# Kernel optimization log

Measured on AMD Instinct MI355X. Metric: run time of the kernel, lower is better.

Reference implementation:

```python
import jax, jax.numpy as jnp
import numpy as np

B, H, S, D = 4, 16, 2048, 64

def setup_inputs() -> dict:
    key = jax.random.key(0)
    kq, kk, kv = jax.random.split(key, 3)
    Q = jax.random.normal(kq, (B, H, S, D), dtype=jnp.float32)
    K = jax.random.normal(kk, (B, H, S, D), dtype=jnp.float32)
    V = jax.random.normal(kv, (B, H, S, D), dtype=jnp.float32)
    return {"Q": Q, "K": K, "V": V}

def reference(Q, K, V):
    d = Q.shape[-1]
    scale = jnp.sqrt(jnp.asarray(d, dtype=Q.dtype))
    # scores: [B, H, S, S]
    scores = jnp.einsum('bhqd,bhkd->bhqk', Q, K) / scale
    attn = jax.nn.softmax(scores, axis=-1)
    out = jnp.einsum('bhqk,bhkd->bhqd', attn, V)  # [B,H,S,D]
    # permute to [B,S,H,D] then merge heads -> [B,S,H*D]
    b, h, s, dd = out.shape
    return out.transpose(0, 2, 1, 3).reshape(b, s, h * dd)
```

## Files before the change

### kernel.cpp

```cpp
#include <hip/hip_runtime.h>
#include <hip/hip_bf16.h>


#define B_ 4
#define H_ 16
#define S_ 2048
#define D_ 64
#define BH 64
#define NKT 32
#define TILE_USH 4096
#define ARR_USH ((size_t)BH * NKT * TILE_USH)
#define WS_NEED (2 * ARR_USH * 2)
#define QSCALE 0.18033688011112042f

typedef float  f4 __attribute__((ext_vector_type(4)));
typedef short  s4 __attribute__((ext_vector_type(4)));
typedef short  s8 __attribute__((ext_vector_type(8)));
typedef unsigned short ushort_t;

__device__ __forceinline__ unsigned short f2bf(float x) {
  unsigned int u = __float_as_uint(x);
  u += 0x7fffu + ((u >> 16) & 1u);
  return (unsigned short)(u >> 16);
}
__device__ __forceinline__ unsigned int pk_bf16(float a, float b) {
  __hip_bfloat162 h = __float22bfloat162_rn(make_float2(a, b));
  union { __hip_bfloat162 h2; unsigned int u; } cv; cv.h2 = h; return cv.u;
}
__device__ __forceinline__ void splitbf_rne(float x, unsigned short& hi, unsigned short& lo) {
  hi = f2bf(x);
  float hf = __uint_as_float((unsigned int)hi << 16);
  lo = f2bf(x - hf);
}
__device__ __forceinline__ void splitbf(float x, unsigned short& hi, unsigned short& lo) {
  unsigned int u = __float_as_uint(x);
  hi = (unsigned short)(u >> 16);
  float hf = __uint_as_float(u & 0xffff0000u);
  lo = (unsigned short)(__float_as_uint(x - hf) >> 16);
}

typedef __attribute__((address_space(1))) const unsigned int* gas_t;
typedef __attribute__((address_space(3))) unsigned int* las_t;
__device__ __forceinline__ void gl_lds16(const void* g, void* l) {
  __builtin_amdgcn_global_load_lds((gas_t)g, (las_t)l, 16, 0, 0);
}

__global__ __launch_bounds__(256)
void prep(const float* __restrict__ K, const float* __restrict__ V,
          ushort_t* __restrict__ KH, ushort_t* __restrict__ VT) {
  __shared__ float Vf[64][68];
  const int tile = blockIdx.x;
  const int t = threadIdx.x;

  const float* vsrc = V + (size_t)tile * 4096;
  float4 vv[4];
  int srow[4], dcol[4];
  #pragma unroll
  for (int r = 0; r < 4; ++r) {
    int f = r * 256 + t; srow[r] = f >> 4; dcol[r] = (f & 15) << 2;
    vv[r] = *(const float4*)(vsrc + srow[r] * 64 + dcol[r]);
  }
  {
    const float* src0 = K + (size_t)tile * 4096;
    #pragma unroll
    for (int u = 0; u < 2; ++u) {
      unsigned int i = u * 256 + t;
      unsigned int row = i >> 3, c = (i & 7) ^ (row & 7);
      const float* src = src0 + row * 64 + c * 8;
      float4 a = *(const float4*)src;
      float4 b = *(const float4*)(src + 4);
      unsigned int d0 = pk_bf16(a.x, a.y), d1 = pk_bf16(a.z, a.w);
      unsigned int d2 = pk_bf16(b.x, b.y), d3 = pk_bf16(b.z, b.w);
      uint4 out = make_uint4(d0, d1, d2, d3);
      *(uint4*)(KH + (size_t)tile * TILE_USH + i * 8) = out;
    }
  }
  #pragma unroll
  for (int r = 0; r < 4; ++r) {
    int pcol = dcol[r] ^ (((srow[r] >> 3) & 3) << 2);
    *(float4*)&Vf[srow[r]][pcol] = vv[r];
  }
  __syncthreads();
  #pragma unroll
  for (int u = 0; u < 2; ++u) {
    unsigned int i = u * 256 + t;
    unsigned int drow = i >> 3, c = (i & 7) ^ (drow & 7);
    const unsigned int col = drow ^ ((c & 3) << 2);
    unsigned int d0 = pk_bf16(Vf[c * 8 + 0][col], Vf[c * 8 + 1][col]);
    unsigned int d1 = pk_bf16(Vf[c * 8 + 2][col], Vf[c * 8 + 3][col]);
    unsigned int d2 = pk_bf16(Vf[c * 8 + 4][col], Vf[c * 8 + 5][col]);
    unsigned int d3 = pk_bf16(Vf[c * 8 + 6][col], Vf[c * 8 + 7][col]);
    uint4 out = make_uint4(d0, d1, d2, d3);
    *(uint4*)(VT + (size_t)tile * TILE_USH + i * 8) = out;
  }
}

__global__ __launch_bounds__(256, 2)
void attn6(const float* __restrict__ Q, const ushort_t* __restrict__ KH,
           const ushort_t* __restrict__ VT, float* __restrict__ O) {
  __shared__ ushort_t KhS[2][TILE_USH];
  __shared__ ushort_t VtS[2][TILE_USH];
  __shared__ ushort_t Pb[4][TILE_USH];

  const int t    = threadIdx.x;
  const int w    = t >> 6;
  const int lane = t & 63;
  const int g    = lane >> 4;
  const int ln   = lane & 15;

  const unsigned int n = blockIdx.x;
  const int bh = (int)((n >> 6) * 8 + (n & 7));
  const int q0 = (int)(((n >> 3) & 7) * 256);

  const size_t tb = (size_t)bh * NKT * TILE_USH;
  const unsigned int cb = w * 128;

  #pragma unroll
  for (int j = 0; j < 2; ++j) {
    const unsigned int ch = cb + 64u * j;
    const size_t go = tb + (size_t)(ch + lane) * 8;
    gl_lds16(KH + go, &KhS[0][ch * 8]);
    gl_lds16(VT + go, &VtS[0][ch * 8]);
  }

  s8 qfh[4][2], qfl[4][2];
  #pragma unroll
  for (int sub = 0; sub < 4; ++sub) {
    const int q = q0 + 64 * w + 16 * sub + ln;
    #pragma unroll
    for (int ks = 0; ks < 2; ++ks) {
      const float* qp = Q + ((size_t)bh * S_ + q) * 64 + 32 * ks + 8 * g;
      float4 a = *(const float4*)qp;
      float4 b = *(const float4*)(qp + 4);
      float xs[8] = {a.x, a.y, a.z, a.w, b.x, b.y, b.z, b.w};
      s8 hv, lv;
      #pragma unroll
      for (int j = 0; j < 8; ++j) {
        unsigned short h, lo; splitbf_rne(xs[j] * QSCALE, h, lo);
        hv[j] = (short)h; lv[j] = (short)lo;
      }
      qfh[sub][ks] = hv; qfl[sub][ks] = lv;
    }
  }

  f4 oacc[4][4];
  f4 lacc[4];
  #pragma unroll
  for (int s = 0; s < 4; ++s) {
    lacc[s] = (f4)0.0f;
    #pragma unroll
    for (int d = 0; d < 4; ++d) oacc[s][d] = (f4)0.0f;
  }

  s8 ones;
  #pragma unroll
  for (int j = 0; j < 8; ++j) ones[j] = (short)0x3F80;

  unsigned int foff[2];
  #pragma unroll
  for (int ks = 0; ks < 2; ++ks)
    foff[ks] = (unsigned)ln * 128u + (unsigned)(((4 * ks + g) ^ (ln & 7)) * 16);

  for (int kt = 0; kt < NKT; ++kt) {
    const int cur = kt & 1;
    __syncthreads();

    if (kt + 1 < NKT) {
      const size_t tbase = tb + (size_t)(kt + 1) * TILE_USH;
      const int nb = cur ^ 1;
      #pragma unroll
      for (int j = 0; j < 2; ++j) {
        const unsigned int ch = cb + 64u * j;
        const size_t go = tbase + (size_t)(ch + lane) * 8;
        gl_lds16(KH + go, &KhS[nb][ch * 8]);
        gl_lds16(VT + go, &VtS[nb][ch * 8]);
      }
    }

    const char* khb = (const char*)&KhS[cur][0];
    const char* vtb = (const char*)&VtS[cur][0];

    #pragma unroll
    for (int nt = 0; nt < 4; ++nt) {
      s8 kh0 = *(const s8*)(khb + nt * 2048 + foff[0]);
      s8 kh1 = *(const s8*)(khb + nt * 2048 + foff[1]);
      #pragma unroll
      for (int sub = 0; sub < 4; ++sub) {
        f4 sc = (f4)0.0f;
        sc = __builtin_amdgcn_mfma_f32_16x16x32_bf16(qfh[sub][0], kh0, sc, 0, 0, 0);
        sc = __builtin_amdgcn_mfma_f32_16x16x32_bf16(qfl[sub][0], kh0, sc, 0, 0, 0);
        sc = __builtin_amdgcn_mfma_f32_16x16x32_bf16(qfh[sub][1], kh1, sc, 0, 0, 0);
        sc = __builtin_amdgcn_mfma_f32_16x16x32_bf16(qfl[sub][1], kh1, sc, 0, 0, 0);
        float p0 = __builtin_amdgcn_exp2f(sc[0]);
        float p1 = __builtin_amdgcn_exp2f(sc[1]);
        float p2 = __builtin_amdgcn_exp2f(sc[2]);
        float p3 = __builtin_amdgcn_exp2f(sc[3]);
        unsigned int pk01 = pk_bf16(p0, p1);
        unsigned int pk23 = pk_bf16(p2, p3);
        const unsigned int c0 = 16u * nt + (unsigned)ln;
        ushort_t* base = &Pb[w][(16 * sub + 4 * g) * 64];
        base[       (c0 ^ (8u * (unsigned)((4 * g + 0) & 7)))] = (ushort_t)pk01;
        base[ 64u + (c0 ^ (8u * (unsigned)((4 * g + 1) & 7)))] = (ushort_t)(pk01 >> 16);
        base[128u + (c0 ^ (8u * (unsigned)((4 * g + 2) & 7)))] = (ushort_t)pk23;
        base[192u + (c0 ^ (8u * (unsigned)((4 * g + 3) & 7)))] = (ushort_t)(pk23 >> 16);
      }
    }

    #pragma unroll
    for (int ks = 0; ks < 2; ++ks) {
      s8 pa[4];
      #pragma unroll
      for (int sub = 0; sub < 4; ++sub) {
        pa[sub] = *(const s8*)((const char*)&Pb[w][0] + sub * 2048 + foff[ks]);
        lacc[sub] = __builtin_amdgcn_mfma_f32_16x16x32_bf16(pa[sub], ones, lacc[sub], 0, 0, 0);
      }
      #pragma unroll
      for (int dt = 0; dt < 4; ++dt) {
        s8 vb = *(const s8*)(vtb + dt * 2048 + foff[ks]);
        #pragma unroll
        for (int sub = 0; sub < 4; ++sub)
          oacc[sub][dt] = __builtin_amdgcn_mfma_f32_16x16x32_bf16(pa[sub], vb, oacc[sub][dt], 0, 0, 0);
      }
    }
  }

  const int b = bh >> 4, h = bh & 15;
  #pragma unroll
  for (int sub = 0; sub < 4; ++sub)
    #pragma unroll
    for (int r = 0; r < 4; ++r) {
      const float inv = 1.0f / lacc[sub][r];
      const int q = q0 + 64 * w + 16 * sub + 4 * g + r;
      float* dst = O + ((size_t)b * S_ + q) * (H_ * D_) + h * 64;
      #pragma unroll
      for (int dt = 0; dt < 4; ++dt)
        dst[16 * dt + ln] = oacc[sub][dt][r] * inv;
    }
}

#define KQ_STR 72
#define VP_STR 76
__global__ __launch_bounds__(256, 2)
void attn_mfma(const float* __restrict__ Q, const float* __restrict__ K,
               const float* __restrict__ V, float* __restrict__ O) {
  __shared__ __align__(16) unsigned short Qh[64][KQ_STR];
  __shared__ __align__(16) unsigned short Ql[64][KQ_STR];
  __shared__ __align__(16) unsigned short Kh[64][KQ_STR];
  __shared__ __align__(16) unsigned short Kl[64][KQ_STR];
  __shared__ __align__(16) unsigned short Vt[64][VP_STR];
  __shared__ __align__(16) unsigned short Pb2[4][16][VP_STR];
  const int t = threadIdx.x, w = t >> 6, lane = t & 63, g = lane >> 4, ln = lane & 15;
  const int bh = blockIdx.x, q0 = blockIdx.y * 64;
  const size_t base = (size_t)bh * S_ * D_;
  {
    const float* Qg = Q + base + (size_t)q0 * D_;
    #pragma unroll
    for (int r = 0; r < 4; ++r) {
      int f = r * 256 + t, row = f >> 4, c4 = (f & 15) << 2;
      float4 v = *(const float4*)(Qg + row * 64 + c4);
      s4 hv, lv; unsigned short hb, lb;
      splitbf(v.x * 0.125f, hb, lb); hv[0] = (short)hb; lv[0] = (short)lb;
      splitbf(v.y * 0.125f, hb, lb); hv[1] = (short)hb; lv[1] = (short)lb;
      splitbf(v.z * 0.125f, hb, lb); hv[2] = (short)hb; lv[2] = (short)lb;
      splitbf(v.w * 0.125f, hb, lb); hv[3] = (short)hb; lv[3] = (short)lb;
      *(s4*)&Qh[row][c4] = hv; *(s4*)&Ql[row][c4] = lv;
    }
  }
  __syncthreads();
  s8 qfh[2], qfl[2];
  #pragma unroll
  for (int ks = 0; ks < 2; ++ks) {
    qfh[ks] = *(const s8*)&Qh[16 * w + ln][ks * 32 + 8 * g];
    qfl[ks] = *(const s8*)&Ql[16 * w + ln][ks * 32 + 8 * g];
  }
  f4 oacc[4]; float m[4], l[4];
  #pragma unroll
  for (int i = 0; i < 4; ++i) { oacc[i] = (f4)0.0f; m[i] = -1e30f; l[i] = 0.0f; }
  const float* Kg = K + base; const float* Vg = V + base;
  float4 kreg[4], vreg[4];
  #pragma unroll
  for (int r = 0; r < 4; ++r) {
    int f = r * 256 + t, row = f >> 4, c4 = (f & 15) << 2;
    kreg[r] = *(const float4*)(Kg + row * 64 + c4);
  }
  #pragma unroll
  for (int j = 0; j < 2; ++j) {
    int it = j * 256 + t, kp = it >> 4, c4 = (it & 15) << 2;
    vreg[2 * j] = *(const float4*)(Vg + (2 * kp) * 64 + c4);
    vreg[2 * j + 1] = *(const float4*)(Vg + (2 * kp + 1) * 64 + c4);
  }
  for (int kt = 0; kt < S_ / 64; ++kt) {
    __syncthreads();
    #pragma unroll
    for (int r = 0; r < 4; ++r) {
      int f = r * 256 + t, row = f >> 4, c4 = (f & 15) << 2;
      float4 v = kreg[r];
      s4 hv, lv; unsigned short hb, lb;
      splitbf(v.x, hb, lb); hv[0] = (short)hb; lv[0] = (short)lb;
      splitbf(v.y, hb, lb); hv[1] = (short)hb; lv[1] = (short)lb;
      splitbf(v.z, hb, lb); hv[2] = (short)hb; lv[2] = (short)lb;
      splitbf(v.w, hb, lb); hv[3] = (short)hb; lv[3] = (short)lb;
      *(s4*)&Kh[row][c4] = hv; *(s4*)&Kl[row][c4] = lv;
    }
    #pragma unroll
    for (int j = 0; j < 2; ++j) {
      int it = j * 256 + t, kp = it >> 4, c4 = (it & 15) << 2;
      float4 a = vreg[2 * j], b = vreg[2 * j + 1];
      float xa[4] = {a.x, a.y, a.z, a.w}, xb[4] = {b.x, b.y, b.z, b.w};
      #pragma unroll
      for (int i = 0; i < 4; ++i) {
        unsigned int pk = (unsigned int)f2bf(xa[i]) | ((unsigned int)f2bf(xb[i]) << 16);
        *(unsigned int*)&Vt[c4 + i][2 * kp] = pk;
      }
    }
    if (kt + 1 < S_ / 64) {
      const float* Kt = Kg + (size_t)(kt + 1) * 4096;
      const float* Vn = Vg + (size_t)(kt + 1) * 4096;
      #pragma unroll
      for (int r = 0; r < 4; ++r) {
        int f = r * 256 + t, row = f >> 4, c4 = (f & 15) << 2;
        kreg[r] = *(const float4*)(Kt + row * 64 + c4);
      }
      #pragma unroll
      for (int j = 0; j < 2; ++j) {
        int it = j * 256 + t, kp = it >> 4, c4 = (it & 15) << 2;
        vreg[2 * j] = *(const float4*)(Vn + (2 * kp) * 64 + c4);
        vreg[2 * j + 1] = *(const float4*)(Vn + (2 * kp + 1) * 64 + c4);
      }
    }
    __syncthreads();
    f4 sacc[4];
    #pragma unroll
    for (int nt = 0; nt < 4; ++nt) sacc[nt] = (f4)0.0f;
    #pragma unroll
    for (int nt = 0; nt < 4; ++nt)
      #pragma unroll
      for (int ks = 0; ks < 2; ++ks) {
        s8 kh = *(const s8*)&Kh[16 * nt + ln][ks * 32 + 8 * g];
        s8 kl = *(const s8*)&Kl[16 * nt + ln][ks * 32 + 8 * g];
        sacc[nt] = __builtin_amdgcn_mfma_f32_16x16x32_bf16(qfh[ks], kh, sacc[nt], 0, 0, 0);
        sacc[nt] = __builtin_amdgcn_mfma_f32_16x16x32_bf16(qfl[ks], kh, sacc[nt], 0, 0, 0);
        sacc[nt] = __builtin_amdgcn_mfma_f32_16x16x32_bf16(qfh[ks], kl, sacc[nt], 0, 0, 0);
      }
    #pragma unroll
    for (int r = 0; r < 4; ++r) {
      float rm = fmaxf(fmaxf(sacc[0][r], sacc[1][r]), fmaxf(sacc[2][r], sacc[3][r]));
      rm = fmaxf(rm, __shfl_xor(rm, 1)); rm = fmaxf(rm, __shfl_xor(rm, 2));
      rm = fmaxf(rm, __shfl_xor(rm, 4)); rm = fmaxf(rm, __shfl_xor(rm, 8));
      float mn = fmaxf(m[r], rm);
      float alpha = __expf(m[r] - mn); m[r] = mn;
      float p0 = __expf(sacc[0][r] - mn), p1 = __expf(sacc[1][r] - mn);
      float p2 = __expf(sacc[2][r] - mn), p3 = __expf(sacc[3][r] - mn);
      float rs = p0 + p1 + p2 + p3;
      rs += __shfl_xor(rs, 1); rs += __shfl_xor(rs, 2);
      rs += __shfl_xor(rs, 4); rs += __shfl_xor(rs, 8);
      l[r] = l[r] * alpha + rs;
      oacc[0][r] *= alpha; oacc[1][r] *= alpha; oacc[2][r] *= alpha; oacc[3][r] *= alpha;
      const int row = 4 * g + r;
      Pb2[w][row][ln] = f2bf(p0); Pb2[w][row][ln + 16] = f2bf(p1);
      Pb2[w][row][ln + 32] = f2bf(p2); Pb2[w][row][ln + 48] = f2bf(p3);
    }
    #pragma unroll
    for (int ks = 0; ks < 2; ++ks) {
      s4 pa0 = *(const s4*)&Pb2[w][ln][ks * 32 + 8 * g];
      s4 pa1 = *(const s4*)&Pb2[w][ln][ks * 32 + 8 * g + 4];
      s8 pa = __builtin_shufflevector(pa0, pa1, 0, 1, 2, 3, 4, 5, 6, 7);
      #pragma unroll
      for (int dt = 0; dt < 4; ++dt) {
        s4 vb0 = *(const s4*)&Vt[16 * dt + ln][ks * 32 + 8 * g];
        s4 vb1 = *(const s4*)&Vt[16 * dt + ln][ks * 32 + 8 * g + 4];
        s8 vb = __builtin_shufflevector(vb0, vb1, 0, 1, 2, 3, 4, 5, 6, 7);
        oacc[dt] = __builtin_amdgcn_mfma_f32_16x16x32_bf16(pa, vb, oacc[dt], 0, 0, 0);
      }
    }
  }
  const int b = bh >> 4, h = bh & 15;
  #pragma unroll
  for (int r = 0; r < 4; ++r) {
    const int q = q0 + 16 * w + 4 * g + r;
    const float inv = 1.0f / l[r];
    float* dst = O + ((size_t)b * S_ + q) * (H_ * D_) + h * 64;
    #pragma unroll
    for (int dt = 0; dt < 4; ++dt) dst[16 * dt + ln] = oacc[dt][r] * inv;
  }
}

extern "C" void kernel_launch(void* const* d_in, const int* in_sizes, int n_in,
                              void* d_out, int out_size, void* d_ws, size_t ws_size,
                              hipStream_t stream) {
  const float* Q = (const float*)d_in[0];
  const float* K = (const float*)d_in[1];
  const float* V = (const float*)d_in[2];
  float* Out = (float*)d_out;
  if (ws_size >= WS_NEED) {
    ushort_t* KHp = (ushort_t*)d_ws;
    ushort_t* VTp = KHp + ARR_USH;
    hipLaunchKernelGGL(prep, dim3(2048), dim3(256), 0, stream, K, V, KHp, VTp);
    hipLaunchKernelGGL(attn6, dim3(512), dim3(256), 0, stream, Q, KHp, VTp, Out);
  } else {
    hipLaunchKernelGGL(attn_mfma, dim3(BH, S_ / 64), dim3(256), 0, stream, Q, K, V, Out);
  }
}
```

Measured before the change: 225.2 us.

## Halve query tile per block and split P staging into 32-key halves for occupancy

Each block now handles 128 queries (32 per wave) instead of 256, so the grid doubles to 1024 blocks and launch bounds allow 4 blocks per CU. The P staging buffer shrinks from 8 KB to 2 KB per wave because each 64-key tile is processed in two 32-key halves, each followed immediately by its PV MFMAs, and it gets a new swizzle. This cuts LDS use and registers to raise occupancy and overlap softmax with PV. In exchange every K/V tile is loaded and converted by twice as many blocks, roughly doubling global/L2 traffic for K and V.

```diff
diff --git a/kernel.cpp b/kernel.cpp
--- a/kernel.cpp
+++ b/kernel.cpp
@@ -95,12 +95,12 @@
   }
 }
 
-__global__ __launch_bounds__(256, 2)
-void attn6(const float* __restrict__ Q, const ushort_t* __restrict__ KH,
+__global__ __launch_bounds__(256, 4)
+void attn7(const float* __restrict__ Q, const ushort_t* __restrict__ KH,
            const ushort_t* __restrict__ VT, float* __restrict__ O) {
   __shared__ ushort_t KhS[2][TILE_USH];
   __shared__ ushort_t VtS[2][TILE_USH];
-  __shared__ ushort_t Pb[4][TILE_USH];
+  __shared__ ushort_t Pb[4][1024];
 
   const int t    = threadIdx.x;
   const int w    = t >> 6;
@@ -109,8 +109,8 @@
   const int ln   = lane & 15;
 
   const unsigned int n = blockIdx.x;
-  const int bh = (int)((n >> 6) * 8 + (n & 7));
-  const int q0 = (int)(((n >> 3) & 7) * 256);
+  const int bh = (int)((n >> 7) * 8 + (n & 7));
+  const int q0 = (int)(((n >> 3) & 15) * 128);
 
   const size_t tb = (size_t)bh * NKT * TILE_USH;
   const unsigned int cb = w * 128;
@@ -123,10 +123,10 @@
     gl_lds16(VT + go, &VtS[0][ch * 8]);
   }
 
-  s8 qfh[4][2], qfl[4][2];
-  #pragma unroll
-  for (int sub = 0; sub < 4; ++sub) {
-    const int q = q0 + 64 * w + 16 * sub + ln;
+  s8 qfh[2][2], qfl[2][2];
+  #pragma unroll
+  for (int sub = 0; sub < 2; ++sub) {
+    const int q = q0 + 32 * w + 16 * sub + ln;
     #pragma unroll
     for (int ks = 0; ks < 2; ++ks) {
       const float* qp = Q + ((size_t)bh * S_ + q) * 64 + 32 * ks + 8 * g;
@@ -143,10 +143,10 @@
     }
   }
 
-  f4 oacc[4][4];
-  f4 lacc[4];
-  #pragma unroll
-  for (int s = 0; s < 4; ++s) {
+  f4 oacc[2][4];
+  f4 lacc[2];
+  #pragma unroll
+  for (int s = 0; s < 2; ++s) {
     lacc[s] = (f4)0.0f;
     #pragma unroll
     for (int d = 0; d < 4; ++d) oacc[s][d] = (f4)0.0f;
@@ -160,6 +160,8 @@
   #pragma unroll
   for (int ks = 0; ks < 2; ++ks)
     foff[ks] = (unsigned)ln * 128u + (unsigned)(((4 * ks + g) ^ (ln & 7)) * 16);
+
+  const unsigned int pro = (unsigned)ln * 64u + (unsigned)((g ^ (ln >> 2)) & 3) * 16u;
 
   for (int kt = 0; kt < NKT; ++kt) {
     const int cur = kt & 1;
@@ -181,57 +183,58 @@
     const char* vtb = (const char*)&VtS[cur][0];
 
     #pragma unroll
-    for (int nt = 0; nt < 4; ++nt) {
-      s8 kh0 = *(const s8*)(khb + nt * 2048 + foff[0]);
-      s8 kh1 = *(const s8*)(khb + nt * 2048 + foff[1]);
-      #pragma unroll
-      for (int sub = 0; sub < 4; ++sub) {
-        f4 sc = (f4)0.0f;
-        sc = __builtin_amdgcn_mfma_f32_16x16x32_bf16(qfh[sub][0], kh0, sc, 0, 0, 0);
-        sc = __builtin_amdgcn_mfma_f32_16x16x32_bf16(qfl[sub][0], kh0, sc, 0, 0, 0);
-        sc = __builtin_amdgcn_mfma_f32_16x16x32_bf16(qfh[sub][1], kh1, sc, 0, 0, 0);
-        sc = __builtin_amdgcn_mfma_f32_16x16x32_bf16(qfl[sub][1], kh1, sc, 0, 0, 0);
-        float p0 = __builtin_amdgcn_exp2f(sc[0]);
-        float p1 = __builtin_amdgcn_exp2f(sc[1]);
-        float p2 = __builtin_amdgcn_exp2f(sc[2]);
-        float p3 = __builtin_amdgcn_exp2f(sc[3]);
-        unsigned int pk01 = pk_bf16(p0, p1);
-        unsigned int pk23 = pk_bf16(p2, p3);
-        const unsigned int c0 = 16u * nt + (unsigned)ln;
-        ushort_t* base = &Pb[w][(16 * sub + 4 * g) * 64];
-        base[       (c0 ^ (8u * (unsigned)((4 * g + 0) & 7)))] = (ushort_t)pk01;
-        base[ 64u + (c0 ^ (8u * (unsigned)((4 * g + 1) & 7)))] = (ushort_t)(pk01 >> 16);
-        base[128u + (c0 ^ (8u * (unsigned)((4 * g + 2) & 7)))] = (ushort_t)pk23;
-        base[192u + (c0 ^ (8u * (unsigned)((4 * g + 3) & 7)))] = (ushort_t)(pk23 >> 16);
-      }
-    }
-
-    #pragma unroll
-    for (int ks = 0; ks < 2; ++ks) {
-      s8 pa[4];
-      #pragma unroll
-      for (int sub = 0; sub < 4; ++sub) {
-        pa[sub] = *(const s8*)((const char*)&Pb[w][0] + sub * 2048 + foff[ks]);
+    for (int h = 0; h < 2; ++h) {
+      #pragma unroll
+      for (int ntl = 0; ntl < 2; ++ntl) {
+        const int nt = 2 * h + ntl;
+        s8 kh0 = *(const s8*)(khb + nt * 2048 + foff[0]);
+        s8 kh1 = *(const s8*)(khb + nt * 2048 + foff[1]);
+        const unsigned int c1 = (16u * (unsigned)ntl + (unsigned)ln) ^ (8u * (unsigned)g);
+        #pragma unroll
+        for (int sub = 0; sub < 2; ++sub) {
+          f4 sc = (f4)0.0f;
+          sc = __builtin_amdgcn_mfma_f32_16x16x32_bf16(qfh[sub][0], kh0, sc, 0, 0, 0);
+          sc = __builtin_amdgcn_mfma_f32_16x16x32_bf16(qfl[sub][0], kh0, sc, 0, 0, 0);
+          sc = __builtin_amdgcn_mfma_f32_16x16x32_bf16(qfh[sub][1], kh1, sc, 0, 0, 0);
+          sc = __builtin_amdgcn_mfma_f32_16x16x32_bf16(qfl[sub][1], kh1, sc, 0, 0, 0);
+          float p0 = __builtin_amdgcn_exp2f(sc[0]);
+          float p1 = __builtin_amdgcn_exp2f(sc[1]);
+          float p2 = __builtin_amdgcn_exp2f(sc[2]);
+          float p3 = __builtin_amdgcn_exp2f(sc[3]);
+          unsigned int pk01 = pk_bf16(p0, p1);
+          unsigned int pk23 = pk_bf16(p2, p3);
+          ushort_t* base = &Pb[w][sub * 512];
+          base[(4 * g + 0) * 32 + c1] = (ushort_t)pk01;
+          base[(4 * g + 1) * 32 + c1] = (ushort_t)(pk01 >> 16);
+          base[(4 * g + 2) * 32 + c1] = (ushort_t)pk23;
+          base[(4 * g + 3) * 32 + c1] = (ushort_t)(pk23 >> 16);
+        }
+      }
+
+      s8 pa[2];
+      #pragma unroll
+      for (int sub = 0; sub < 2; ++sub) {
+        pa[sub] = *(const s8*)((const char*)&Pb[w][0] + sub * 1024 + pro);
         lacc[sub] = __builtin_amdgcn_mfma_f32_16x16x32_bf16(pa[sub], ones, lacc[sub], 0, 0, 0);
       }
       #pragma unroll
       for (int dt = 0; dt < 4; ++dt) {
-        s8 vb = *(const s8*)(vtb + dt * 2048 + foff[ks]);
+        s8 vb = *(const s8*)(vtb + dt * 2048 + foff[h]);
         #pragma unroll
-        for (int sub = 0; sub < 4; ++sub)
+        for (int sub = 0; sub < 2; ++sub)
           oacc[sub][dt] = __builtin_amdgcn_mfma_f32_16x16x32_bf16(pa[sub], vb, oacc[sub][dt], 0, 0, 0);
       }
     }
   }
 
-  const int b = bh >> 4, h = bh & 15;
-  #pragma unroll
-  for (int sub = 0; sub < 4; ++sub)
+  const int b = bh >> 4, hh = bh & 15;
+  #pragma unroll
+  for (int sub = 0; sub < 2; ++sub)
     #pragma unroll
     for (int r = 0; r < 4; ++r) {
       const float inv = 1.0f / lacc[sub][r];
-      const int q = q0 + 64 * w + 16 * sub + 4 * g + r;
-      float* dst = O + ((size_t)b * S_ + q) * (H_ * D_) + h * 64;
+      const int q = q0 + 32 * w + 16 * sub + 4 * g + r;
+      float* dst = O + ((size_t)b * S_ + q) * (H_ * D_) + hh * 64;
       #pragma unroll
       for (int dt = 0; dt < 4; ++dt)
         dst[16 * dt + ln] = oacc[sub][dt][r] * inv;
@@ -396,7 +399,7 @@
     ushort_t* KHp = (ushort_t*)d_ws;
     ushort_t* VTp = KHp + ARR_USH;
     hipLaunchKernelGGL(prep, dim3(2048), dim3(256), 0, stream, K, V, KHp, VTp);
-    hipLaunchKernelGGL(attn6, dim3(512), dim3(256), 0, stream, Q, KHp, VTp, Out);
+    hipLaunchKernelGGL(attn7, dim3(1024), dim3(256), 0, stream, Q, KHp, VTp, Out);
   } else {
     hipLaunchKernelGGL(attn_mfma, dim3(BH, S_ / 64), dim3(256), 0, stream, Q, K, V, Out);
   }
```

Measured after the change: 221.5 us. About the same (-1.6%).
